# Optimization experiments

Hardware: AMD Instinct MI355X
Metric: run time of the kernel (lower is better)

## Reference

```python
import jax, jax.numpy as jnp
import numpy as np

K = 7          # kernel_size from init
PAD = (K - 1) // 2
EPS = 1e-8


def _local_std(x):
    """Per-pixel std of the zero-padded KxK x C neighborhood, matching
    torch: unfold(pad=3) -> mean over dim=1 (C*K*K) -> sqrt(mean(d^2)+eps).
    Computed with box-filter convolutions instead of materializing the
    49x-blown-up unfold tensor.
    Returns [B, H*W].
    """
    B, C, H, W = x.shape
    n = C * K * K  # fixed divisor (zero padding counts toward the mean)
    ones = jnp.ones((1, C, K, K), x.dtype)  # OIHW: sums over channels + window
    s = jax.lax.conv_general_dilated(x, ones, (1, 1), [(PAD, PAD), (PAD, PAD)])      # [B,1,H,W]
    s2 = jax.lax.conv_general_dilated(x * x, ones, (1, 1), [(PAD, PAD), (PAD, PAD)])  # [B,1,H,W]
    mu = s / n
    var = s2 / n - mu * mu  # E[x^2] - mu^2 == mean((x-mu)^2)
    return jnp.sqrt(var + EPS).reshape(B, H * W)


def _smooth_l1_mean(a, b):
    d = a - b
    ad = jnp.abs(d)
    per = jnp.where(ad < 1.0, 0.5 * d * d, ad - 0.5)
    return jnp.mean(per)


def setup_inputs() -> dict:
    key = jax.random.key(0)
    k1, k2 = jax.random.split(key)
    shape = (16, 3, 512, 512)
    pred_moire = jax.random.normal(k1, shape, dtype=jnp.float32)
    moire = jax.random.normal(k2, shape, dtype=jnp.float32)
    return {"pred_moire": pred_moire, "moire": moire}


def reference(pred_moire, moire):
    std_pred = _local_std(pred_moire)  # [B, H*W]
    std_tgt = _local_std(moire)        # [B, H*W]
    return _smooth_l1_mean(std_pred, std_tgt)  # scalar
```

## Files before the change

kernel.cpp:

```cpp
#include <hip/hip_runtime.h>


typedef float f32x4 __attribute__((ext_vector_type(4)));

#define K     7
#define PAD   3
#define TSX   64
#define TSY   32
#define HR    (TSY + K - 1)
#define LDSW  64
#define NT    256
#define NTASK (2 * HR * 8)

#define LOADQ(dst, ptr, OFF)                                        \
    asm volatile("global_load_dwordx4 %0, %1, off offset:" OFF      \
                 : "=v"(dst) : "v"(ptr))

#define WAITV(N) do {                                               \
    asm volatile("s_waitcnt vmcnt(" #N ")" ::: "memory");           \
    __builtin_amdgcn_sched_barrier(0);                              \
} while (0)

__global__ __launch_bounds__(NT, 4) void dist_loss_kernel(
    const float* __restrict__ pred,
    const float* __restrict__ tgt,
    float* __restrict__ out)
{
    constexpr int   C = 3, H = 512, W = 512;
    constexpr float INV_N     = 1.0f / (C * K * K);
    constexpr float INV_TOTAL = 1.0f / (16.0f * 512.0f * 512.0f);

    __shared__ float sh_s[2][HR][LDSW];
    __shared__ float sh_q[2][HR][LDSW];

    const int    tid  = threadIdx.x;
    const int    tx0  = blockIdx.x * TSX;
    const int    ty0  = blockIdx.y * TSY;
    const int    b    = blockIdx.z;
    const size_t plane = (size_t)H * W;
    const size_t planeB = plane * sizeof(float);

    const float* base0 = pred + (size_t)b * C * plane;
    const float* base1 = tgt  + (size_t)b * C * plane;

    float* shs = &sh_s[0][0][0];
    float* shq = &sh_q[0][0][0];

    #define DECL_SLOT(S)                                                     \
        const char *rB0_##S, *rB1_##S, *rB2_##S;                             \
        int cA_##S, cE_##S, idx_##S;                                         \
        float m_##S, mL_##S, mR_##S;                                         \
        f32x4 qA0_##S, qB0_##S, qD0_##S, qE0_##S,                            \
              qA1_##S, qB1_##S, qD1_##S, qE1_##S,                            \
              qA2_##S, qB2_##S, qD2_##S, qE2_##S;

    #define SETUP(S, t) do {                                                 \
        const int which = ((t) >= HR * 8) ? 1 : 0;                           \
        const int tt    = (t) - which * (HR * 8);                            \
        const int row   = tt >> 3, cg = tt & 7;                              \
        const int gy    = ty0 - PAD + row;                                   \
        m_##S  = ((unsigned)gy < (unsigned)H) ? 1.f : 0.f;                   \
        const int gyc = min(max(gy, 0), H - 1);                              \
        const int gx0 = tx0 + (cg << 3);                                     \
        mL_##S = (gx0 > 0)   ? 1.f : 0.f;                                    \
        mR_##S = (gx0 < 504) ? 1.f : 0.f;                                    \
        const float* base = which ? base1 : base0;                           \
        rB0_##S = (const char*)(base + (size_t)gyc * W + gx0);               \
        rB1_##S = rB0_##S + planeB;                                          \
        rB2_##S = rB1_##S + planeB;                                          \
        cA_##S  = (gx0 > 0)   ? -16 : 0;                                     \
        cE_##S  = (gx0 < 504) ?  32 : 16;                                    \
        idx_##S = (which * HR + row) * LDSW + (cg << 3);                     \
    } while (0)

    #define ISSUE(S) do {                                                    \
        LOADQ(qA0_##S, rB0_##S + cA_##S, "0");                               \
        LOADQ(qB0_##S, rB0_##S,          "0");                               \
        LOADQ(qD0_##S, rB0_##S,          "16");                              \
        LOADQ(qE0_##S, rB0_##S + cE_##S, "0");                               \
        LOADQ(qA1_##S, rB1_##S + cA_##S, "0");                               \
        LOADQ(qB1_##S, rB1_##S,          "0");                               \
        LOADQ(qD1_##S, rB1_##S,          "16");                              \
        LOADQ(qE1_##S, rB1_##S + cE_##S, "0");                               \
        LOADQ(qA2_##S, rB2_##S + cA_##S, "0");                               \
        LOADQ(qB2_##S, rB2_##S,          "0");                               \
        LOADQ(qD2_##S, rB2_##S,          "16");                              \
        LOADQ(qE2_##S, rB2_##S + cE_##S, "0");                               \
    } while (0)

    #define CONSUME(S) do {                                                  \
        f32x4 tl = qA0_##S + qA1_##S + qA2_##S;                              \
        f32x4 ta = qB0_##S + qB1_##S + qB2_##S;                              \
        f32x4 tb = qD0_##S + qD1_##S + qD2_##S;                              \
        f32x4 tr = qE0_##S + qE1_##S + qE2_##S;                              \
        f32x4 ul = qA0_##S*qA0_##S + qA1_##S*qA1_##S + qA2_##S*qA2_##S;      \
        f32x4 ua = qB0_##S*qB0_##S + qB1_##S*qB1_##S + qB2_##S*qB2_##S;      \
        f32x4 ub = qD0_##S*qD0_##S + qD1_##S*qD1_##S + qD2_##S*qD2_##S;      \
        f32x4 ur = qE0_##S*qE0_##S + qE1_##S*qE1_##S + qE2_##S*qE2_##S;      \
        tl[1] *= mL_##S; tl[2] *= mL_##S; tl[3] *= mL_##S;                   \
        ul[1] *= mL_##S; ul[2] *= mL_##S; ul[3] *= mL_##S;                   \
        tr[0] *= mR_##S; tr[1] *= mR_##S; tr[2] *= mR_##S;                   \
        ur[0] *= mR_##S; ur[1] *= mR_##S; ur[2] *= mR_##S;                   \
        float h0 = tl[1]+tl[2]+tl[3]+ta[0]+ta[1]+ta[2]+ta[3];                \
        float h1 = h0 - tl[1] + tb[0];                                       \
        float h2 = h1 - tl[2] + tb[1];                                       \
        float h3 = h2 - tl[3] + tb[2];                                       \
        float h4 = h3 - ta[0] + tb[3];                                       \
        float h5 = h4 - ta[1] + tr[0];                                       \
        float h6 = h5 - ta[2] + tr[1];                                       \
        float h7 = h6 - ta[3] + tr[2];                                       \
        float g0 = ul[1]+ul[2]+ul[3]+ua[0]+ua[1]+ua[2]+ua[3];                \
        float g1 = g0 - ul[1] + ub[0];                                       \
        float g2 = g1 - ul[2] + ub[1];                                       \
        float g3 = g2 - ul[3] + ub[2];                                       \
        float g4 = g3 - ua[0] + ub[3];                                       \
        float g5 = g4 - ua[1] + ur[0];                                       \
        float g6 = g5 - ua[2] + ur[1];                                       \
        float g7 = g6 - ua[3] + ur[2];                                       \
        const float mm = m_##S;                                              \
        *(f32x4*)&shs[idx_##S]     = (f32x4){h0*mm, h1*mm, h2*mm, h3*mm};    \
        *(f32x4*)&shs[idx_##S + 4] = (f32x4){h4*mm, h5*mm, h6*mm, h7*mm};    \
        *(f32x4*)&shq[idx_##S]     = (f32x4){g0*mm, g1*mm, g2*mm, g3*mm};    \
        *(f32x4*)&shq[idx_##S + 4] = (f32x4){g4*mm, g5*mm, g6*mm, g7*mm};    \
    } while (0)

    DECL_SLOT(0);
    DECL_SLOT(1);
    const int t0 = tid;
    const int t1 = tid + NT;
    const int t2 = min(tid + 2 * NT, NTASK - 1);

    SETUP(0, t0); ISSUE(0);
    SETUP(1, t1); ISSUE(1);
    WAITV(12);
    CONSUME(0);
    SETUP(0, t2); ISSUE(0);
    WAITV(12);
    CONSUME(1);
    WAITV(0);
    CONSUME(0);

    __syncthreads();

    float acc = 0.0f;
    {
        const int rp = tid >> 4;
        const int x  = (tid & 15) << 2;

        f32x4 pA, pB;

        #define STD4(Sv, Qv, D) do {                                         \
            _Pragma("unroll")                                                \
            for (int c_ = 0; c_ < 4; ++c_) {                                 \
                float mu_ = (Sv)[c_] * INV_N;                                \
                (D)[c_] = sqrtf(fmaf(-mu_, mu_, (Qv)[c_] * INV_N) + 1e-8f);  \
            }                                                                \
        } while (0)
        #define SL1(a, bb) do {                                              \
            float d_  = (a) - (bb);                                          \
            float ad_ = fabsf(d_);                                           \
            acc += (ad_ < 1.0f) ? 0.5f * d_ * d_ : (ad_ - 0.5f);             \
        } while (0)

        #pragma unroll
        for (int w = 0; w < 2; ++w) {
            f32x4 S = (f32x4){0.f, 0.f, 0.f, 0.f};
            f32x4 Q = (f32x4){0.f, 0.f, 0.f, 0.f};
            #pragma unroll
            for (int k = 0; k < K; ++k) {
                S += *(const f32x4*)&sh_s[w][2 * rp + k][x];
                Q += *(const f32x4*)&sh_q[w][2 * rp + k][x];
            }
            f32x4 S2 = S - *(const f32x4*)&sh_s[w][2 * rp][x]
                         + *(const f32x4*)&sh_s[w][2 * rp + 7][x];
            f32x4 Q2 = Q - *(const f32x4*)&sh_q[w][2 * rp][x]
                         + *(const f32x4*)&sh_q[w][2 * rp + 7][x];

            if (w == 0) {
                STD4(S, Q, pA);
                STD4(S2, Q2, pB);
            } else {
                f32x4 sA, sB;
                STD4(S, Q, sA);
                STD4(S2, Q2, sB);
                SL1(pA[0], sA[0]); SL1(pA[1], sA[1]);
                SL1(pA[2], sA[2]); SL1(pA[3], sA[3]);
                SL1(pB[0], sB[0]); SL1(pB[1], sB[1]);
                SL1(pB[2], sB[2]); SL1(pB[3], sB[3]);
            }
        }
        #undef STD4
        #undef SL1
    }

    #pragma unroll
    for (int off = 32; off > 0; off >>= 1)
        acc += __shfl_down(acc, off, 64);

    __shared__ float wave_sums[NT / 64];
    if ((tid & 63) == 0) wave_sums[tid >> 6] = acc;
    __syncthreads();
    if (tid == 0) {
        float s = 0.0f;
        #pragma unroll
        for (int w = 0; w < NT / 64; ++w) s += wave_sums[w];
        atomicAdd(out, s * INV_TOTAL);
    }
}

extern "C" void kernel_launch(void* const* d_in, const int* in_sizes, int n_in,
                              void* d_out, int out_size, void* d_ws, size_t ws_size,
                              hipStream_t stream) {
    const float* pred = (const float*)d_in[0];
    const float* tgt  = (const float*)d_in[1];
    float* out = (float*)d_out;

    hipMemsetAsync(out, 0, sizeof(float), stream);

    dim3 grid(512 / TSX, 512 / TSY, 16);
    dist_loss_kernel<<<grid, NT, 0, stream>>>(pred, tgt, out);
}
```

Baseline: 129.4 us.

## Halve tile height to 16 rows and simplify load pipeline for higher occupancy

Tile height drops from 32 to 16 rows, so each thread computes one output row instead of two and the horizontal-pass load schedule shrinks from a two-slot, three-task pipeline to one slot with an optional second task. Fewer live registers and less LDS per block allow the launch bound to rise from 4 to 5 blocks per SIMD-group, aiming to hide memory latency through occupancy instead of explicit software pipelining. In exchange the 6-row vertical halo is now amortised over 16 rows rather than 32, so redundant global loads and horizontal work grow by roughly 40% per output, and each load is waited on fully before it is consumed.

```diff
diff --git a/kernel.cpp b/kernel.cpp
--- a/kernel.cpp
+++ b/kernel.cpp
@@ -6,11 +6,12 @@
 #define K     7
 #define PAD   3
 #define TSX   64
-#define TSY   32
+#define TSY   16
 #define HR    (TSY + K - 1)
 #define LDSW  64
 #define NT    256
-#define NTASK (2 * HR * 8)
+#define HALF  (HR * 8)
+#define NTASK (2 * HALF)
 
 #define LOADQ(dst, ptr, OFF)                                        \
     asm volatile("global_load_dwordx4 %0, %1, off offset:" OFF      \
@@ -21,7 +22,7 @@
     __builtin_amdgcn_sched_barrier(0);                              \
 } while (0)
 
-__global__ __launch_bounds__(NT, 4) void dist_loss_kernel(
+__global__ __launch_bounds__(NT, 5) void dist_loss_kernel(
     const float* __restrict__ pred,
     const float* __restrict__ tgt,
     float* __restrict__ out)
@@ -37,7 +38,7 @@
     const int    tx0  = blockIdx.x * TSX;
     const int    ty0  = blockIdx.y * TSY;
     const int    b    = blockIdx.z;
-    const size_t plane = (size_t)H * W;
+    const size_t plane  = (size_t)H * W;
     const size_t planeB = plane * sizeof(float);
 
     const float* base0 = pred + (size_t)b * C * plane;
@@ -55,8 +56,8 @@
               qA2_##S, qB2_##S, qD2_##S, qE2_##S;
 
     #define SETUP(S, t) do {                                                 \
-        const int which = ((t) >= HR * 8) ? 1 : 0;                           \
-        const int tt    = (t) - which * (HR * 8);                            \
+        const int which = ((t) >= HALF) ? 1 : 0;                             \
+        const int tt    = (t) - which * HALF;                                \
         const int row   = tt >> 3, cg = tt & 7;                              \
         const int gy    = ty0 - PAD + row;                                   \
         m_##S  = ((unsigned)gy < (unsigned)H) ? 1.f : 0.f;                   \
@@ -125,29 +126,24 @@
     } while (0)
 
     DECL_SLOT(0);
-    DECL_SLOT(1);
-    const int t0 = tid;
-    const int t1 = tid + NT;
-    const int t2 = min(tid + 2 * NT, NTASK - 1);
-
-    SETUP(0, t0); ISSUE(0);
-    SETUP(1, t1); ISSUE(1);
-    WAITV(12);
-    CONSUME(0);
-    SETUP(0, t2); ISSUE(0);
-    WAITV(12);
-    CONSUME(1);
+
+    SETUP(0, tid); ISSUE(0);
     WAITV(0);
     CONSUME(0);
+    if (tid < NTASK - NT) {
+        SETUP(0, tid + NT); ISSUE(0);
+        WAITV(0);
+        CONSUME(0);
+    }
 
     __syncthreads();
 
     float acc = 0.0f;
     {
-        const int rp = tid >> 4;
-        const int x  = (tid & 15) << 2;
-
-        f32x4 pA, pB;
+        const int r = tid >> 4;
+        const int x = (tid & 15) << 2;
+
+        f32x4 pA;
 
         #define STD4(Sv, Qv, D) do {                                         \
             _Pragma("unroll")                                                \
@@ -168,25 +164,16 @@
             f32x4 Q = (f32x4){0.f, 0.f, 0.f, 0.f};
             #pragma unroll
             for (int k = 0; k < K; ++k) {
-                S += *(const f32x4*)&sh_s[w][2 * rp + k][x];
-                Q += *(const f32x4*)&sh_q[w][2 * rp + k][x];
+                S += *(const f32x4*)&sh_s[w][r + k][x];
+                Q += *(const f32x4*)&sh_q[w][r + k][x];
             }
-            f32x4 S2 = S - *(const f32x4*)&sh_s[w][2 * rp][x]
-                         + *(const f32x4*)&sh_s[w][2 * rp + 7][x];
-            f32x4 Q2 = Q - *(const f32x4*)&sh_q[w][2 * rp][x]
-                         + *(const f32x4*)&sh_q[w][2 * rp + 7][x];
-
             if (w == 0) {
                 STD4(S, Q, pA);
-                STD4(S2, Q2, pB);
             } else {
-                f32x4 sA, sB;
+                f32x4 sA;
                 STD4(S, Q, sA);
-                STD4(S2, Q2, sB);
                 SL1(pA[0], sA[0]); SL1(pA[1], sA[1]);
                 SL1(pA[2], sA[2]); SL1(pA[3], sA[3]);
-                SL1(pB[0], sB[0]); SL1(pB[1], sB[1]);
-                SL1(pB[2], sB[2]); SL1(pB[3], sB[3]);
             }
         }
         #undef STD4
```

Result: slower. 154.5 us (+19.4%).
